# Optimization experiments

Measured on AMD Instinct MI355X. Metric: run time of the kernel, lower is better.

Reference implementation:

```python
import jax, jax.numpy as jnp
import numpy as np
import math

D = 512      # input_size == hidden_size
TAU = 4      # length of att/spatial lists
N = 16384    # tokens (batch*H*W)

def setup_inputs() -> dict:
    key = jax.random.key(0)
    ks = jax.random.split(key, 16)
    s = 1.0 / math.sqrt(D)
    return {
        "T_t": jax.random.normal(ks[0], (N, D), jnp.float32),
        "S_t": jax.random.normal(ks[1], (N, D), jnp.float32),
        "t_att": jax.random.normal(ks[2], (TAU, N, D), jnp.float32),
        "s_att": jax.random.normal(ks[3], (TAU, N, D), jnp.float32),
        "t_spatial": jax.random.normal(ks[4], (TAU, N, D), jnp.float32),
        "s_spatial": jax.random.normal(ks[5], (TAU, N, D), jnp.float32),
        # fl_t: Linear(D, 3D); fl_t_next: Linear(D, D); same for s
        "W_t": jax.random.uniform(ks[6], (3 * D, D), jnp.float32, -s, s),
        "b_t": jax.random.uniform(ks[7], (3 * D,), jnp.float32, -s, s),
        "W_tn": jax.random.uniform(ks[8], (D, D), jnp.float32, -s, s),
        "b_tn": jax.random.uniform(ks[9], (D,), jnp.float32, -s, s),
        "W_s": jax.random.uniform(ks[10], (3 * D, D), jnp.float32, -s, s),
        "b_s": jax.random.uniform(ks[11], (3 * D,), jnp.float32, -s, s),
        "W_sn": jax.random.uniform(ks[12], (D, D), jnp.float32, -s, s),
        "b_sn": jax.random.uniform(ks[13], (D,), jnp.float32, -s, s),
    }

def reference(T_t, S_t, t_att, s_att, t_spatial, s_spatial,
              W_t, b_t, W_tn, b_tn, W_s, b_s, W_sn, b_sn):
    d = T_t.shape[-1]
    scale = 1.0 / jnp.sqrt(jnp.asarray(d, T_t.dtype))
    s_next = S_t @ W_sn.T + b_sn          # [N, D]
    t_next = T_t @ W_tn.T + b_tn          # [N, D]

    # trend weights: dot-product along feature dim, softmax over tau axis
    w_s = jax.nn.softmax(jnp.einsum('knd,nd->kn', s_att, s_next) * scale, axis=0)
    w_t = jax.nn.softmax(jnp.einsum('knd,nd->kn', t_spatial, t_next) * scale, axis=0)
    T_trend = jnp.einsum('knd,kn->nd', t_att, w_s)      # [N, D]
    S_trend = jnp.einsum('knd,kn->nd', s_spatial, w_t)  # [N, D]

    t_gate = jax.nn.sigmoid(t_next)
    s_gate = jax.nn.sigmoid(s_next)
    T_fusion = T_t * t_gate + (1.0 - t_gate) * T_trend
    S_fusion = S_t * s_gate + (1.0 - s_gate) * S_trend

    T_concat = T_fusion @ W_t.T + b_t     # [N, 3D]
    S_concat = S_fusion @ W_s.T + b_s
    t_g, t_t, t_s = jnp.split(T_concat, 3, axis=1)
    s_g, s_t, s_s = jnp.split(S_concat, 3, axis=1)
    T_gate = jax.nn.sigmoid(t_g)
    S_gate = jax.nn.sigmoid(s_g)
    T_new = T_gate * t_t + (1.0 - T_gate) * s_t
    S_new = S_gate * s_s + (1.0 - S_gate) * t_s
    return T_new, S_new
```

## Files before the change

kernel.cpp:

```cpp
#include <hip/hip_runtime.h>

#define NTOK 16384
#define DIM 512
#define NTAU 4

typedef __attribute__((ext_vector_type(4))) float f32x4;
typedef __attribute__((ext_vector_type(8))) short bf16x8;
typedef __attribute__((ext_vector_type(4))) unsigned short u16x4;
typedef __attribute__((ext_vector_type(8))) unsigned short u16x8;
typedef unsigned int u32;

__device__ inline unsigned short f2bf(float f) {
    union { float f; unsigned int u; } v; v.f = f;
    unsigned int u = v.u + 0x7FFFu + ((v.u >> 16) & 1u);
    return (unsigned short)(u >> 16);
}

__device__ inline void bf8_to_f32(u16x8 h, f32x4& a, f32x4& b) {
    union { unsigned int u; float f; } t;
#pragma unroll
    for (int e = 0; e < 4; e++) { t.u = ((unsigned int)h[e]) << 16; a[e] = t.f; }
#pragma unroll
    for (int e = 0; e < 4; e++) { t.u = ((unsigned int)h[4 + e]) << 16; b[e] = t.f; }
}

#define NTLOAD4(p) __builtin_nontemporal_load((const f32x4*)(p))

__device__ __forceinline__ void gload16(const void* g, void* l) {
    __builtin_amdgcn_global_load_lds((const __attribute__((address_space(1))) u32*)g,
                                     (__attribute__((address_space(3))) u32*)l, 16, 0, 0);
}

__global__ void convert_all(const float* __restrict__ a, const float* __restrict__ b,
                            const float* __restrict__ c, const float* __restrict__ d,
                            unsigned short* __restrict__ oa, unsigned short* __restrict__ ob,
                            unsigned short* __restrict__ oc, unsigned short* __restrict__ od) {
    int i = blockIdx.x * 256 + threadIdx.x;
    const float* s; unsigned short* t; int off;
    if (i < 65536)       { s = a; t = oa; off = i; }
    else if (i < 131072) { s = b; t = ob; off = i - 65536; }
    else if (i < 327680) { s = c; t = oc; off = i - 131072; }
    else                 { s = d; t = od; off = i - 327680; }
    f32x4 v = ((const f32x4*)s)[off];
    u16x4 o;
    o[0] = f2bf(v[0]); o[1] = f2bf(v[1]); o[2] = f2bf(v[2]); o[3] = f2bf(v[3]);
    ((u16x4*)t)[off] = o;
}

__global__ __launch_bounds__(256, 2) void gemm_next2(
    const float* __restrict__ T_t, const float* __restrict__ S_t,
    const unsigned short* __restrict__ Wtn, const unsigned short* __restrict__ Wsn,
    const float* __restrict__ btn, const float* __restrict__ bsn,
    unsigned short* __restrict__ t_next, unsigned short* __restrict__ s_next)
{
    __shared__ unsigned short lA[128][40];
    __shared__ unsigned short lB[128][40];
    const int tid = threadIdx.x;
    const int id = blockIdx.x;
    const int xcd = id & 7;
    const int rest = id >> 3;
    const int mat = rest & 1;
    const int idx = rest >> 1;
    const float* A = mat ? S_t : T_t;
    const unsigned short* W = mat ? Wsn : Wtn;
    const float* bias = mat ? bsn : btn;
    unsigned short* out = mat ? s_next : t_next;
    const int m0 = (xcd * 16 + (idx >> 2)) * 128;
    const int n0 = (idx & 3) * 128;
    const int lane = tid & 63;
    const int w = tid >> 6;
    const int wr = w >> 1, wc = w & 1;

    f32x4 acc[4][4];
#pragma unroll
    for (int i = 0; i < 4; i++)
#pragma unroll
        for (int j = 0; j < 4; j++) acc[i][j] = (f32x4){0.f, 0.f, 0.f, 0.f};

    const int arow = tid >> 3;
    const int acol = (tid & 7) * 4;
    const int brow = tid >> 2;
    const int bcol = (tid & 3) * 8;

    for (int k0 = 0; k0 < DIM; k0 += 32) {
#pragma unroll
        for (int i = 0; i < 4; i++) {
            int r = arow + 32 * i;
            f32x4 v = *(const f32x4*)(A + (size_t)(m0 + r) * DIM + k0 + acol);
            u16x4 o;
            o[0] = f2bf(v[0]); o[1] = f2bf(v[1]); o[2] = f2bf(v[2]); o[3] = f2bf(v[3]);
            *(u16x4*)&lA[r][acol] = o;
        }
#pragma unroll
        for (int i = 0; i < 2; i++) {
            int r = brow + 64 * i;
            u16x8 v = *(const u16x8*)(W + (size_t)(n0 + r) * DIM + k0 + bcol);
            *(u16x8*)&lB[r][bcol] = v;
        }
        __syncthreads();

        bf16x8 af[4], bfr[4];
#pragma unroll
        for (int i = 0; i < 4; i++)
            af[i] = *(const bf16x8*)&lA[wr * 64 + i * 16 + (lane & 15)][(lane >> 4) * 8];
#pragma unroll
        for (int j = 0; j < 4; j++)
            bfr[j] = *(const bf16x8*)&lB[wc * 64 + j * 16 + (lane & 15)][(lane >> 4) * 8];
#pragma unroll
        for (int i = 0; i < 4; i++)
#pragma unroll
            for (int j = 0; j < 4; j++)
                acc[i][j] = __builtin_amdgcn_mfma_f32_16x16x32_bf16(af[i], bfr[j], acc[i][j], 0, 0, 0);
        __syncthreads();
    }

#pragma unroll
    for (int j = 0; j < 4; j++) {
        int n = n0 + wc * 64 + j * 16 + (lane & 15);
        float bv = bias[n];
#pragma unroll
        for (int i = 0; i < 4; i++) {
            int mbase = m0 + wr * 64 + i * 16 + (lane >> 4) * 4;
#pragma unroll
            for (int r = 0; r < 4; r++)
                out[(size_t)(mbase + r) * DIM + n] = f2bf(acc[i][j][r] + bv);
        }
    }
}

__global__ __launch_bounds__(256) void dots_kernel(
    const float* __restrict__ s_att, const float* __restrict__ t_spatial,
    const unsigned short* __restrict__ t_next, const unsigned short* __restrict__ s_next,
    float* __restrict__ w_all)
{
    const int lane = threadIdx.x & 63;
    const int id = blockIdx.x;
    const int n = (id & 7) * 2048 + (id >> 3) * 4 + (threadIdx.x >> 6);
    const int c = lane * 8;
    const size_t rb = (size_t)n * DIM + c;
    const float scale = 0.04419417382415922f;

    f32x4 tn_a, tn_b, sn_a, sn_b;
    bf8_to_f32(*(const u16x8*)(t_next + rb), tn_a, tn_b);
    bf8_to_f32(*(const u16x8*)(s_next + rb), sn_a, sn_b);

    float dws[NTAU], dwt[NTAU];
#pragma unroll
    for (int k = 0; k < NTAU; k++) {
        const size_t kb = ((size_t)k * NTOK + n) * DIM + c;
        f32x4 a0 = NTLOAD4(s_att + kb);
        f32x4 a1 = NTLOAD4(s_att + kb + 4);
        f32x4 b0 = NTLOAD4(t_spatial + kb);
        f32x4 b1 = NTLOAD4(t_spatial + kb + 4);
        dws[k] = a0[0]*sn_a[0]+a0[1]*sn_a[1]+a0[2]*sn_a[2]+a0[3]*sn_a[3]
               + a1[0]*sn_b[0]+a1[1]*sn_b[1]+a1[2]*sn_b[2]+a1[3]*sn_b[3];
        dwt[k] = b0[0]*tn_a[0]+b0[1]*tn_a[1]+b0[2]*tn_a[2]+b0[3]*tn_a[3]
               + b1[0]*tn_b[0]+b1[1]*tn_b[1]+b1[2]*tn_b[2]+b1[3]*tn_b[3];
    }
#pragma unroll
    for (int k = 0; k < NTAU; k++) {
        float v = dws[k];
#pragma unroll
        for (int off = 32; off; off >>= 1) v += __shfl_xor(v, off);
        dws[k] = v * scale;
        float u = dwt[k];
#pragma unroll
        for (int off = 32; off; off >>= 1) u += __shfl_xor(u, off);
        dwt[k] = u * scale;
    }

    float ms = fmaxf(fmaxf(dws[0], dws[1]), fmaxf(dws[2], dws[3]));
    float mt = fmaxf(fmaxf(dwt[0], dwt[1]), fmaxf(dwt[2], dwt[3]));
    f32x4 wsv, wtv;
    float ssum = 0.f, tsum = 0.f;
#pragma unroll
    for (int k = 0; k < NTAU; k++) {
        wsv[k] = __expf(dws[k] - ms); ssum += wsv[k];
        wtv[k] = __expf(dwt[k] - mt); tsum += wtv[k];
    }
    float rs = 1.f / ssum, rt = 1.f / tsum;
#pragma unroll
    for (int k = 0; k < NTAU; k++) { wsv[k] *= rs; wtv[k] *= rt; }

    if (lane == 0) {
        *(f32x4*)(w_all + (size_t)n * 8)     = wsv;
        *(f32x4*)(w_all + (size_t)n * 8 + 4) = wtv;
    }
}

__global__ __launch_bounds__(256) void fusion_kernel(
    const float* __restrict__ T_t, const float* __restrict__ S_t,
    const float* __restrict__ t_att, const float* __restrict__ s_spatial,
    const unsigned short* __restrict__ t_next, const unsigned short* __restrict__ s_next,
    const float* __restrict__ w_all,
    unsigned short* __restrict__ Tf, unsigned short* __restrict__ Sf)
{
    const int lane = threadIdx.x & 63;
    const int id = blockIdx.x;
    const int n = (id & 7) * 2048 + (id >> 3) * 4 + (threadIdx.x >> 6);
    const int c = lane * 8;
    const size_t rb = (size_t)n * DIM + c;

    f32x4 wsv = *(const f32x4*)(w_all + (size_t)n * 8);
    f32x4 wtv = *(const f32x4*)(w_all + (size_t)n * 8 + 4);

    f32x4 Tta = {0,0,0,0}, Ttb = {0,0,0,0}, Sta = {0,0,0,0}, Stb = {0,0,0,0};
#pragma unroll
    for (int k = 0; k < NTAU; k++) {
        const size_t kb = ((size_t)k * NTOK + n) * DIM + c;
        f32x4 ta = NTLOAD4(t_att + kb);
        f32x4 tb = NTLOAD4(t_att + kb + 4);
        f32x4 sa = NTLOAD4(s_spatial + kb);
        f32x4 sb = NTLOAD4(s_spatial + kb + 4);
        float wk = wsv[k], vk = wtv[k];
#pragma unroll
        for (int e = 0; e < 4; e++) {
            Tta[e] += wk * ta[e]; Ttb[e] += wk * tb[e];
            Sta[e] += vk * sa[e]; Stb[e] += vk * sb[e];
        }
    }

    f32x4 tn_a, tn_b, sn_a, sn_b;
    bf8_to_f32(*(const u16x8*)(t_next + rb), tn_a, tn_b);
    bf8_to_f32(*(const u16x8*)(s_next + rb), sn_a, sn_b);
    f32x4 Ta = NTLOAD4(T_t + rb);
    f32x4 Tb = NTLOAD4(T_t + rb + 4);
    f32x4 Sa = NTLOAD4(S_t + rb);
    f32x4 Sb = NTLOAD4(S_t + rb + 4);

    u16x8 oT, oS;
#pragma unroll
    for (int e = 0; e < 4; e++) {
        float gt_a = 1.f / (1.f + __expf(-tn_a[e]));
        float gt_b = 1.f / (1.f + __expf(-tn_b[e]));
        float gs_a = 1.f / (1.f + __expf(-sn_a[e]));
        float gs_b = 1.f / (1.f + __expf(-sn_b[e]));
        oT[e]     = f2bf(Ta[e] * gt_a + (1.f - gt_a) * Tta[e]);
        oT[4 + e] = f2bf(Tb[e] * gt_b + (1.f - gt_b) * Ttb[e]);
        oS[e]     = f2bf(Sa[e] * gs_a + (1.f - gs_a) * Sta[e]);
        oS[4 + e] = f2bf(Sb[e] * gs_b + (1.f - gs_b) * Stb[e]);
    }
    *(u16x8*)(Tf + rb) = oT;
    *(u16x8*)(Sf + rb) = oS;
}

__global__ __launch_bounds__(512, 2) void gemm_final(
    const unsigned short* __restrict__ Tf, const unsigned short* __restrict__ Sf,
    const unsigned short* __restrict__ Wt, const unsigned short* __restrict__ Ws,
    const float* __restrict__ bt, const float* __restrict__ bs,
    float* __restrict__ out)
{
    __shared__ __align__(16) unsigned char smem[32768];
    const int tid = threadIdx.x;
    const int id = blockIdx.x;
    const int xcd = id & 7;
    const int idx = id >> 3;
    const int m0 = (xcd * 16 + (idx >> 4)) * 128;
    const int j0 = (idx & 15) * 32;
    const int lane = tid & 63;
    const int w = tid >> 6;
    const int side = w >> 2;
    const int mh = (w >> 1) & 1;
    const int jq = w & 1;

    f32x4 acc[3][4];
#pragma unroll
    for (int g = 0; g < 3; g++)
#pragma unroll
        for (int i = 0; i < 4; i++) acc[g][i] = (f32x4){0.f, 0.f, 0.f, 0.f};

    const int srow = lane >> 2;
    const int sg   = lane & 3;

    const unsigned short* gsrc[2];
    int dsto[2];
#pragma unroll
    for (int i = 0; i < 2; i++) {
        const int ch = w * 2 + i;
        const unsigned short* base = (ch < 8) ? Tf : Sf;
        const int row = (ch & 7) * 16 + srow;
        const int lg = sg ^ ((row >> 1) & 3);
        gsrc[i] = base + (size_t)(m0 + row) * DIM + lg * 8;
        dsto[i] = ch * 1024;
    }

    int axo[4];
#pragma unroll
    for (int i = 0; i < 4; i++) {
        const int row = mh * 64 + i * 16 + (lane & 15);
        const int pg = (lane >> 4) ^ ((row >> 1) & 3);
        axo[i] = side * 8192 + row * 64 + pg * 16;
    }

    const unsigned short* Wm = side ? Ws : Wt;
    const int jcol = j0 + jq * 16 + (lane & 15);
    const unsigned short* bp[3];
#pragma unroll
    for (int g = 0; g < 3; g++)
        bp[g] = Wm + (size_t)(g * 512 + jcol) * DIM + (lane >> 4) * 8;

    auto stageA = [&](int buf) {
#pragma unroll
        for (int i = 0; i < 2; i++)
            gload16(gsrc[i], smem + buf * 16384 + dsto[i]);
    };

    bf16x8 bcur[3], bnxt[3];
    stageA(0);
#pragma unroll
    for (int g = 0; g < 3; g++) bcur[g] = *(const bf16x8*)(bp[g]);
#pragma unroll
    for (int i = 0; i < 2; i++) gsrc[i] += 32;
#pragma unroll
    for (int g = 0; g < 3; g++) bp[g] += 32;
    __syncthreads();

    int cur = 0;
    for (int kt = 0; kt < 16; ++kt) {
        if (kt < 15) {
            stageA(cur ^ 1);
#pragma unroll
            for (int g = 0; g < 3; g++) bnxt[g] = *(const bf16x8*)(bp[g]);
#pragma unroll
            for (int i = 0; i < 2; i++) gsrc[i] += 32;
#pragma unroll
            for (int g = 0; g < 3; g++) bp[g] += 32;
        }

        const unsigned char* abase = smem + cur * 16384;
        bf16x8 ax[4];
#pragma unroll
        for (int i = 0; i < 4; i++) ax[i] = *(const bf16x8*)(abase + axo[i]);
#pragma unroll
        for (int g = 0; g < 3; g++)
#pragma unroll
            for (int i = 0; i < 4; i++)
                acc[g][i] = __builtin_amdgcn_mfma_f32_16x16x32_bf16(ax[i], bcur[g], acc[g][i], 0, 0, 0);

        __syncthreads();
#pragma unroll
        for (int g = 0; g < 3; g++) bcur[g] = bnxt[g];
        cur ^= 1;
    }

    const float* bb = side ? bs : bt;
    const float bg   = bb[jcol];
    const float bown = side ? bb[1024 + jcol] : bb[512 + jcol];
    const float bex  = side ? bb[512 + jcol]  : bb[1024 + jcol];
    float* exf = (float*)smem;
#pragma unroll
    for (int i = 0; i < 4; i++) {
        f32x4 v = side ? acc[1][i] : acc[2][i];
        v[0] += bex; v[1] += bex; v[2] += bex; v[3] += bex;
        *(f32x4*)(exf + ((w * 4 + i) * 64 + lane) * 4) = v;
    }
    __syncthreads();

    float* obase = out + (side ? (size_t)NTOK * DIM : 0);
#pragma unroll
    for (int i = 0; i < 4; i++) {
        f32x4 oth = *(const f32x4*)(exf + (((w ^ 4) * 4 + i) * 64 + lane) * 4);
        f32x4 own = side ? acc[2][i] : acc[1][i];
#pragma unroll
        for (int r = 0; r < 4; r++) {
            const float gate = 1.f / (1.f + __expf(-(acc[0][i][r] + bg)));
            obase[(size_t)(m0 + mh * 64 + i * 16 + (lane >> 4) * 4 + r) * DIM + jcol]
                = gate * (own[r] + bown) + (1.f - gate) * oth[r];
        }
    }
}

extern "C" void kernel_launch(void* const* d_in, const int* in_sizes, int n_in,
                              void* d_out, int out_size, void* d_ws, size_t ws_size,
                              hipStream_t stream) {
    const float* T_t       = (const float*)d_in[0];
    const float* S_t       = (const float*)d_in[1];
    const float* t_att     = (const float*)d_in[2];
    const float* s_att     = (const float*)d_in[3];
    const float* t_spatial = (const float*)d_in[4];
    const float* s_spatial = (const float*)d_in[5];
    const float* W_t  = (const float*)d_in[6];
    const float* b_t  = (const float*)d_in[7];
    const float* W_tn = (const float*)d_in[8];
    const float* b_tn = (const float*)d_in[9];
    const float* W_s  = (const float*)d_in[10];
    const float* b_s  = (const float*)d_in[11];
    const float* W_sn = (const float*)d_in[12];
    const float* b_sn = (const float*)d_in[13];
    float* out = (float*)d_out;

    char* ws = (char*)d_ws;
    unsigned short* t_next = (unsigned short*)(ws + 0);
    unsigned short* s_next = (unsigned short*)(ws + 16777216);
    unsigned short* Tf     = (unsigned short*)(ws + 33554432);
    unsigned short* Sf     = (unsigned short*)(ws + 50331648);
    unsigned short* Wtn_b  = (unsigned short*)(ws + 67108864);
    unsigned short* Wsn_b  = (unsigned short*)(ws + 67633152);
    unsigned short* Wt_b   = (unsigned short*)(ws + 68157440);
    unsigned short* Ws_b   = (unsigned short*)(ws + 69730304);
    float*          w_all  = (float*)(ws + 71303168);

    convert_all<<<2048, 256, 0, stream>>>(W_tn, W_sn, W_t, W_s,
                                          Wtn_b, Wsn_b, Wt_b, Ws_b);

    gemm_next2<<<1024, 256, 0, stream>>>(T_t, S_t, Wtn_b, Wsn_b, b_tn, b_sn,
                                         t_next, s_next);

    dots_kernel<<<4096, 256, 0, stream>>>(s_att, t_spatial, t_next, s_next, w_all);

    fusion_kernel<<<4096, 256, 0, stream>>>(T_t, S_t, t_att, s_spatial,
                                            t_next, s_next, w_all, Tf, Sf);

    gemm_final<<<2048, 512, 0, stream>>>(Tf, Sf, Wt_b, Ws_b, b_t, b_s, out);
}
```

Measured before the change: 321.5 us.

## Stage weights through LDS with a 4-slot async pipeline in final GEMM

The final GEMM block tile shrinks from 128 to 64 rows, and the grid doubles to 4096 blocks. The weight operand is now staged into LDS with async global-to-LDS loads alongside the activations, instead of being loaded directly into registers. A 4-slot ring buffer with explicit vmcnt waits and a single barrier per k-step replaces the double buffer that needed two syncs. This aims to hide global latency and raise occupancy, at the cost of 80KB of LDS per block and halved reuse of the weight tiles.

```diff
diff --git a/kernel.cpp b/kernel.cpp
--- a/kernel.cpp
+++ b/kernel.cpp
@@ -250,121 +250,130 @@
     const float* __restrict__ bt, const float* __restrict__ bs,
     float* __restrict__ out)
 {
-    __shared__ __align__(16) unsigned char smem[32768];
+    __shared__ __align__(16) unsigned char smem[81920];
     const int tid = threadIdx.x;
     const int id = blockIdx.x;
     const int xcd = id & 7;
     const int idx = id >> 3;
-    const int m0 = (xcd * 16 + (idx >> 4)) * 128;
+    const int m0 = (xcd * 32 + (idx >> 4)) * 64;
     const int j0 = (idx & 15) * 32;
     const int lane = tid & 63;
     const int w = tid >> 6;
     const int side = w >> 2;
     const int mh = (w >> 1) & 1;
     const int jq = w & 1;
-
-    f32x4 acc[3][4];
+    const bool w4 = (w < 4);
+
+    f32x4 acc[3][2];
 #pragma unroll
     for (int g = 0; g < 3; g++)
 #pragma unroll
-        for (int i = 0; i < 4; i++) acc[g][i] = (f32x4){0.f, 0.f, 0.f, 0.f};
+        for (int i = 0; i < 2; i++) acc[g][i] = (f32x4){0.f, 0.f, 0.f, 0.f};
 
     const int srow = lane >> 2;
     const int sg   = lane & 3;
-
-    const unsigned short* gsrc[2];
-    int dsto[2];
+    const int lg   = sg ^ ((srow >> 1) & 3);
+
+    const unsigned short* gsrc[3];
+    int dsto[3];
+#pragma unroll
+    for (int i = 0; i < 3; i++) {
+        const int ch = w + i * 8;
+        dsto[i] = ch * 1024;
+        const unsigned short* p = Tf;
+        if (ch < 4) {
+            p = Tf + (size_t)(m0 + ch * 16 + srow) * DIM + lg * 8;
+        } else if (ch < 8) {
+            p = Sf + (size_t)(m0 + (ch - 4) * 16 + srow) * DIM + lg * 8;
+        } else if (ch < 20) {
+            const int r = (ch - 8) * 16 + srow;
+            const int g = r >> 5;
+            const unsigned short* src = (g < 3) ? Wt : Ws;
+            const int wrow = (g < 3 ? g : g - 3) * DIM + j0 + (r & 31);
+            p = src + (size_t)wrow * DIM + lg * 8;
+        }
+        gsrc[i] = p;
+    }
+
+    const int pg = (lane >> 4) ^ (((lane & 15) >> 1) & 3);
+    int axo[2], bwo[3];
 #pragma unroll
     for (int i = 0; i < 2; i++) {
-        const int ch = w * 2 + i;
-        const unsigned short* base = (ch < 8) ? Tf : Sf;
-        const int row = (ch & 7) * 16 + srow;
-        const int lg = sg ^ ((row >> 1) & 3);
-        gsrc[i] = base + (size_t)(m0 + row) * DIM + lg * 8;
-        dsto[i] = ch * 1024;
-    }
-
-    int axo[4];
-#pragma unroll
-    for (int i = 0; i < 4; i++) {
-        const int row = mh * 64 + i * 16 + (lane & 15);
-        const int pg = (lane >> 4) ^ ((row >> 1) & 3);
-        axo[i] = side * 8192 + row * 64 + pg * 16;
-    }
-
-    const unsigned short* Wm = side ? Ws : Wt;
+        const int row = side * 64 + mh * 32 + i * 16 + (lane & 15);
+        axo[i] = row * 64 + pg * 16;
+    }
+#pragma unroll
+    for (int g = 0; g < 3; g++) {
+        const int r = (side * 3 + g) * 32 + jq * 16 + (lane & 15);
+        bwo[g] = 8192 + r * 64 + pg * 16;
+    }
+
+    auto stage = [&](int slot) {
+        unsigned char* dbase = smem + slot * 20480;
+#pragma unroll
+        for (int i = 0; i < 3; i++) {
+            if (i < 2 || w4) {
+                gload16(gsrc[i], dbase + dsto[i]);
+                gsrc[i] += 32;
+            }
+        }
+    };
+
+    stage(0);
+    stage(1);
+
+    for (int kt = 0; kt < 16; ++kt) {
+        if (kt < 14) stage((kt + 2) & 3);
+
+        if (kt < 14) {
+            if (w4) asm volatile("s_waitcnt vmcnt(6)" ::: "memory");
+            else    asm volatile("s_waitcnt vmcnt(4)" ::: "memory");
+        } else if (kt == 14) {
+            if (w4) asm volatile("s_waitcnt vmcnt(3)" ::: "memory");
+            else    asm volatile("s_waitcnt vmcnt(2)" ::: "memory");
+        } else {
+            asm volatile("s_waitcnt vmcnt(0)" ::: "memory");
+        }
+        __builtin_amdgcn_s_barrier();
+        __builtin_amdgcn_sched_barrier(0);
+
+        const unsigned char* base = smem + (kt & 3) * 20480;
+        bf16x8 ax[2], bw[3];
+#pragma unroll
+        for (int i = 0; i < 2; i++) ax[i] = *(const bf16x8*)(base + axo[i]);
+#pragma unroll
+        for (int g = 0; g < 3; g++) bw[g] = *(const bf16x8*)(base + bwo[g]);
+#pragma unroll
+        for (int g = 0; g < 3; g++)
+#pragma unroll
+            for (int i = 0; i < 2; i++)
+                acc[g][i] = __builtin_amdgcn_mfma_f32_16x16x32_bf16(ax[i], bw[g], acc[g][i], 0, 0, 0);
+    }
+    __syncthreads();
+
     const int jcol = j0 + jq * 16 + (lane & 15);
-    const unsigned short* bp[3];
-#pragma unroll
-    for (int g = 0; g < 3; g++)
-        bp[g] = Wm + (size_t)(g * 512 + jcol) * DIM + (lane >> 4) * 8;
-
-    auto stageA = [&](int buf) {
-#pragma unroll
-        for (int i = 0; i < 2; i++)
-            gload16(gsrc[i], smem + buf * 16384 + dsto[i]);
-    };
-
-    bf16x8 bcur[3], bnxt[3];
-    stageA(0);
-#pragma unroll
-    for (int g = 0; g < 3; g++) bcur[g] = *(const bf16x8*)(bp[g]);
-#pragma unroll
-    for (int i = 0; i < 2; i++) gsrc[i] += 32;
-#pragma unroll
-    for (int g = 0; g < 3; g++) bp[g] += 32;
-    __syncthreads();
-
-    int cur = 0;
-    for (int kt = 0; kt < 16; ++kt) {
-        if (kt < 15) {
-            stageA(cur ^ 1);
-#pragma unroll
-            for (int g = 0; g < 3; g++) bnxt[g] = *(const bf16x8*)(bp[g]);
-#pragma unroll
-            for (int i = 0; i < 2; i++) gsrc[i] += 32;
-#pragma unroll
-            for (int g = 0; g < 3; g++) bp[g] += 32;
-        }
-
-        const unsigned char* abase = smem + cur * 16384;
-        bf16x8 ax[4];
-#pragma unroll
-        for (int i = 0; i < 4; i++) ax[i] = *(const bf16x8*)(abase + axo[i]);
-#pragma unroll
-        for (int g = 0; g < 3; g++)
-#pragma unroll
-            for (int i = 0; i < 4; i++)
-                acc[g][i] = __builtin_amdgcn_mfma_f32_16x16x32_bf16(ax[i], bcur[g], acc[g][i], 0, 0, 0);
-
-        __syncthreads();
-#pragma unroll
-        for (int g = 0; g < 3; g++) bcur[g] = bnxt[g];
-        cur ^= 1;
-    }
-
     const float* bb = side ? bs : bt;
     const float bg   = bb[jcol];
     const float bown = side ? bb[1024 + jcol] : bb[512 + jcol];
     const float bex  = side ? bb[512 + jcol]  : bb[1024 + jcol];
     float* exf = (float*)smem;
 #pragma unroll
-    for (int i = 0; i < 4; i++) {
+    for (int i = 0; i < 2; i++) {
         f32x4 v = side ? acc[1][i] : acc[2][i];
         v[0] += bex; v[1] += bex; v[2] += bex; v[3] += bex;
-        *(f32x4*)(exf + ((w * 4 + i) * 64 + lane) * 4) = v;
+        *(f32x4*)(exf + ((w * 2 + i) * 64 + lane) * 4) = v;
     }
     __syncthreads();
 
     float* obase = out + (side ? (size_t)NTOK * DIM : 0);
 #pragma unroll
-    for (int i = 0; i < 4; i++) {
-        f32x4 oth = *(const f32x4*)(exf + (((w ^ 4) * 4 + i) * 64 + lane) * 4);
+    for (int i = 0; i < 2; i++) {
+        f32x4 oth = *(const f32x4*)(exf + (((w ^ 4) * 2 + i) * 64 + lane) * 4);
         f32x4 own = side ? acc[2][i] : acc[1][i];
 #pragma unroll
         for (int r = 0; r < 4; r++) {
             const float gate = 1.f / (1.f + __expf(-(acc[0][i][r] + bg)));
-            obase[(size_t)(m0 + mh * 64 + i * 16 + (lane >> 4) * 4 + r) * DIM + jcol]
+            obase[(size_t)(m0 + mh * 32 + i * 16 + (lane >> 4) * 4 + r) * DIM + jcol]
                 = gate * (own[r] + bown) + (1.f - gate) * oth[r];
         }
     }
@@ -411,5 +420,5 @@
     fusion_kernel<<<4096, 256, 0, stream>>>(T_t, S_t, t_att, s_spatial,
                                             t_next, s_next, w_all, Tf, Sf);
 
-    gemm_final<<<2048, 512, 0, stream>>>(Tf, Sf, Wt_b, Ws_b, b_t, b_s, out);
-}
+    gemm_final<<<4096, 512, 0, stream>>>(Tf, Sf, Wt_b, Ws_b, b_t, b_s, out);
+}
```

Result: faster. 292.0 us (-9.2%).

## Pre-permute final GEMM weights and deepen A-tile pipeline to four LDS stages

Applied to the files above, without the earlier changes.

The fusion-output GEMM's weight matrices are now converted to bf16 in a fragment-major layout, so each lane's B operand becomes one contiguous coalesced 16-byte load instead of a strided row read. The A-tile staging changes from double buffering with __syncthreads to a four-slot LDS ring filled two iterations ahead. Each iteration uses explicit vmcnt waits plus a raw s_barrier, so loads overlap MFMA work. LDS per block doubles to 64KB, which may limit occupancy, and the hand-tuned vmcnt counts are fragile.

```diff
diff --git a/kernel.cpp b/kernel.cpp
--- a/kernel.cpp
+++ b/kernel.cpp
@@ -31,20 +31,37 @@
                                      (__attribute__((address_space(3))) u32*)l, 16, 0, 0);
 }
 
-__global__ void convert_all(const float* __restrict__ a, const float* __restrict__ b,
-                            const float* __restrict__ c, const float* __restrict__ d,
-                            unsigned short* __restrict__ oa, unsigned short* __restrict__ ob,
-                            unsigned short* __restrict__ oc, unsigned short* __restrict__ od) {
+__global__ void convert2(const float* __restrict__ a, const float* __restrict__ b,
+                         unsigned short* __restrict__ oa, unsigned short* __restrict__ ob) {
     int i = blockIdx.x * 256 + threadIdx.x;
-    const float* s; unsigned short* t; int off;
-    if (i < 65536)       { s = a; t = oa; off = i; }
-    else if (i < 131072) { s = b; t = ob; off = i - 65536; }
-    else if (i < 327680) { s = c; t = oc; off = i - 131072; }
-    else                 { s = d; t = od; off = i - 327680; }
+    const float* s = (i < 65536) ? a : b;
+    unsigned short* t = (i < 65536) ? oa : ob;
+    int off = (i < 65536) ? i : i - 65536;
     f32x4 v = ((const f32x4*)s)[off];
     u16x4 o;
     o[0] = f2bf(v[0]); o[1] = f2bf(v[1]); o[2] = f2bf(v[2]); o[3] = f2bf(v[3]);
     ((u16x4*)t)[off] = o;
+}
+
+__global__ void convert_perm(const float* __restrict__ Wt, const float* __restrict__ Ws,
+                             unsigned short* __restrict__ Wtp, unsigned short* __restrict__ Wsp) {
+    int i = blockIdx.x * 256 + threadIdx.x;
+    const float* src = (i < 98304) ? Wt : Ws;
+    unsigned short* dst = (i < 98304) ? Wtp : Wsp;
+    int r = (i < 98304) ? i : i - 98304;
+    int g    = r >> 15;
+    int rem  = r & 32767;
+    int j16  = rem >> 10;
+    int rem2 = rem & 1023;
+    int ks   = rem2 >> 6;
+    int lane = rem2 & 63;
+    int row = g * 512 + j16 * 16 + (lane & 15);
+    int col = ks * 32 + (lane >> 4) * 8;
+    const float* sp = src + (size_t)row * DIM + col;
+    u16x8 o;
+#pragma unroll
+    for (int e = 0; e < 8; e++) o[e] = f2bf(sp[e]);
+    *(u16x8*)(dst + (size_t)r * 8) = o;
 }
 
 __global__ __launch_bounds__(256, 2) void gemm_next2(
@@ -246,11 +263,11 @@
 
 __global__ __launch_bounds__(512, 2) void gemm_final(
     const unsigned short* __restrict__ Tf, const unsigned short* __restrict__ Sf,
-    const unsigned short* __restrict__ Wt, const unsigned short* __restrict__ Ws,
+    const unsigned short* __restrict__ Wtp, const unsigned short* __restrict__ Wsp,
     const float* __restrict__ bt, const float* __restrict__ bs,
     float* __restrict__ out)
 {
-    __shared__ __align__(16) unsigned char smem[32768];
+    __shared__ __align__(16) unsigned char smem[65536];
     const int tid = threadIdx.x;
     const int id = blockIdx.x;
     const int xcd = id & 7;
@@ -271,78 +288,68 @@
 
     const int srow = lane >> 2;
     const int sg   = lane & 3;
-
-    const unsigned short* gsrc[2];
-    int dsto[2];
-#pragma unroll
-    for (int i = 0; i < 2; i++) {
-        const int ch = w * 2 + i;
-        const unsigned short* base = (ch < 8) ? Tf : Sf;
-        const int row = (ch & 7) * 16 + srow;
-        const int lg = sg ^ ((row >> 1) & 3);
-        gsrc[i] = base + (size_t)(m0 + row) * DIM + lg * 8;
-        dsto[i] = ch * 1024;
-    }
-
+    const int lg   = sg ^ ((srow >> 1) & 3);
+
+    const unsigned short* gsrc0 = Tf + (size_t)(m0 + w * 16 + srow) * DIM + lg * 8;
+    const unsigned short* gsrc1 = Sf + (size_t)(m0 + w * 16 + srow) * DIM + lg * 8;
+    const int dst0 = w * 1024;
+    const int dst1 = 8192 + w * 1024;
+
+    const int pg = (lane >> 4) ^ (((lane & 15) >> 1) & 3);
     int axo[4];
 #pragma unroll
-    for (int i = 0; i < 4; i++) {
-        const int row = mh * 64 + i * 16 + (lane & 15);
-        const int pg = (lane >> 4) ^ ((row >> 1) & 3);
-        axo[i] = side * 8192 + row * 64 + pg * 16;
-    }
-
-    const unsigned short* Wm = side ? Ws : Wt;
-    const int jcol = j0 + jq * 16 + (lane & 15);
+    for (int i = 0; i < 4; i++)
+        axo[i] = side * 8192 + (mh * 4 + i) * 1024 + (lane & 15) * 64 + pg * 16;
+
+    const unsigned short* Wp = side ? Wsp : Wtp;
+    const int j16 = (idx & 15) * 2 + jq;
     const unsigned short* bp[3];
 #pragma unroll
     for (int g = 0; g < 3; g++)
-        bp[g] = Wm + (size_t)(g * 512 + jcol) * DIM + (lane >> 4) * 8;
-
-    auto stageA = [&](int buf) {
-#pragma unroll
-        for (int i = 0; i < 2; i++)
-            gload16(gsrc[i], smem + buf * 16384 + dsto[i]);
+        bp[g] = Wp + ((size_t)(g * 32 + j16) * 16) * 512 + lane * 8;
+
+    auto stage = [&](int slot) {
+        unsigned char* d = smem + slot * 16384;
+        gload16(gsrc0, d + dst0); gsrc0 += 32;
+        gload16(gsrc1, d + dst1); gsrc1 += 32;
     };
 
     bf16x8 bcur[3], bnxt[3];
-    stageA(0);
-#pragma unroll
-    for (int g = 0; g < 3; g++) bcur[g] = *(const bf16x8*)(bp[g]);
-#pragma unroll
-    for (int i = 0; i < 2; i++) gsrc[i] += 32;
-#pragma unroll
-    for (int g = 0; g < 3; g++) bp[g] += 32;
-    __syncthreads();
-
-    int cur = 0;
+    stage(0);
+    stage(1);
+#pragma unroll
+    for (int g = 0; g < 3; g++) { bcur[g] = *(const bf16x8*)bp[g]; bp[g] += 512; }
+
     for (int kt = 0; kt < 16; ++kt) {
+        if (kt < 14) stage((kt + 2) & 3);
         if (kt < 15) {
-            stageA(cur ^ 1);
-#pragma unroll
-            for (int g = 0; g < 3; g++) bnxt[g] = *(const bf16x8*)(bp[g]);
-#pragma unroll
-            for (int i = 0; i < 2; i++) gsrc[i] += 32;
-#pragma unroll
-            for (int g = 0; g < 3; g++) bp[g] += 32;
-        }
-
-        const unsigned char* abase = smem + cur * 16384;
+#pragma unroll
+            for (int g = 0; g < 3; g++) { bnxt[g] = *(const bf16x8*)bp[g]; bp[g] += 512; }
+        }
+        if (kt == 0)       asm volatile("s_waitcnt vmcnt(4)" ::: "memory");
+        else if (kt < 14)  asm volatile("s_waitcnt vmcnt(10)" ::: "memory");
+        else if (kt == 14) asm volatile("s_waitcnt vmcnt(8)" ::: "memory");
+        else               asm volatile("s_waitcnt vmcnt(3)" ::: "memory");
+        __builtin_amdgcn_s_barrier();
+        __builtin_amdgcn_sched_barrier(0);
+
+        const unsigned char* base = smem + (kt & 3) * 16384;
         bf16x8 ax[4];
 #pragma unroll
-        for (int i = 0; i < 4; i++) ax[i] = *(const bf16x8*)(abase + axo[i]);
+        for (int i = 0; i < 4; i++) ax[i] = *(const bf16x8*)(base + axo[i]);
 #pragma unroll
         for (int g = 0; g < 3; g++)
 #pragma unroll
             for (int i = 0; i < 4; i++)
                 acc[g][i] = __builtin_amdgcn_mfma_f32_16x16x32_bf16(ax[i], bcur[g], acc[g][i], 0, 0, 0);
-
-        __syncthreads();
-#pragma unroll
-        for (int g = 0; g < 3; g++) bcur[g] = bnxt[g];
-        cur ^= 1;
-    }
-
+        if (kt < 15) {
+#pragma unroll
+            for (int g = 0; g < 3; g++) bcur[g] = bnxt[g];
+        }
+    }
+    __syncthreads();
+
+    const int jcol = j0 + jq * 16 + (lane & 15);
     const float* bb = side ? bs : bt;
     const float bg   = bb[jcol];
     const float bown = side ? bb[1024 + jcol] : bb[512 + jcol];
@@ -396,12 +403,12 @@
     unsigned short* Sf     = (unsigned short*)(ws + 50331648);
     unsigned short* Wtn_b  = (unsigned short*)(ws + 67108864);
     unsigned short* Wsn_b  = (unsigned short*)(ws + 67633152);
-    unsigned short* Wt_b   = (unsigned short*)(ws + 68157440);
-    unsigned short* Ws_b   = (unsigned short*)(ws + 69730304);
+    unsigned short* Wtp    = (unsigned short*)(ws + 68157440);
+    unsigned short* Wsp    = (unsigned short*)(ws + 69730304);
     float*          w_all  = (float*)(ws + 71303168);
 
-    convert_all<<<2048, 256, 0, stream>>>(W_tn, W_sn, W_t, W_s,
-                                          Wtn_b, Wsn_b, Wt_b, Ws_b);
+    convert2<<<512, 256, 0, stream>>>(W_tn, W_sn, Wtn_b, Wsn_b);
+    convert_perm<<<768, 256, 0, stream>>>(W_t, W_s, Wtp, Wsp);
 
     gemm_next2<<<1024, 256, 0, stream>>>(T_t, S_t, Wtn_b, Wsn_b, b_tn, b_sn,
                                          t_next, s_next);
@@ -411,5 +418,5 @@
     fusion_kernel<<<4096, 256, 0, stream>>>(T_t, S_t, t_att, s_spatial,
                                             t_next, s_next, w_all, Tf, Sf);
 
-    gemm_final<<<2048, 512, 0, stream>>>(Tf, Sf, Wt_b, Ws_b, b_t, b_s, out);
-}
+    gemm_final<<<2048, 512, 0, stream>>>(Tf, Sf, Wtp, Wsp, b_t, b_s, out);
+}
```

After: 296.4 us. 1.08x faster.
